# Kernel optimization log

Measured on AMD Instinct MI355X. Metric: run time of the kernel, lower is better.

Reference implementation:

```python
import jax, jax.numpy as jnp
import numpy as np

DEPTH_REF = jnp.array([28.01, 16.32], dtype=jnp.float32)
DIM_REF = jnp.array([[3.88, 1.63, 1.53], [0.84, 1.76, 0.66], [1.78, 1.52, 1.78]], dtype=jnp.float32)
TOPK = 50
DET_THRESHOLD = 0.25
PI = 3.14159265358979


def nms_hm(heat, kernel=3):
    # 3x3 max-pool NMS: keep peaks, zero everything else
    pad = (kernel - 1) // 2
    hmax = jax.lax.reduce_window(heat, -jnp.inf, jax.lax.max,
                                 (1, 1, kernel, kernel), (1, 1, 1, 1),
                                 [(0, 0), (0, 0), (pad, pad), (pad, pad)])
    return jnp.where(hmax == heat, heat, 0.0)


def select_topk(heat, K):
    B, C, H, W = heat.shape
    scores_all, inds_all = jax.lax.top_k(heat.reshape(B, C, H * W), K)  # [B,C,K]
    ys_all = (inds_all // W).astype(jnp.float32)
    xs_all = (inds_all % W).astype(jnp.float32)
    scores, inds = jax.lax.top_k(scores_all.reshape(B, C * K), K)       # [B,K] over classes
    clses = (inds // K).astype(jnp.float32)
    topk_inds = jnp.take_along_axis(inds_all.reshape(B, C * K), inds, axis=1)
    ys = jnp.take_along_axis(ys_all.reshape(B, C * K), inds, axis=1)
    xs = jnp.take_along_axis(xs_all.reshape(B, C * K), inds, axis=1)
    return scores, topk_inds, clses, ys, xs


def select_point_of_interest(index, feature_maps):
    B, Cf, H, W = feature_maps.shape
    fm = feature_maps.transpose(0, 2, 3, 1).reshape(B, H * W, Cf)
    return jnp.take_along_axis(fm, index[:, :, None], axis=1)  # [B,K,Cf]


def encode_box3d(rotys, dims, locs):
    # dims = (l, h, w); corner signs reproduce SMOKE's gather pattern
    N = rotys.shape[0]
    c, s = jnp.cos(rotys), jnp.sin(rotys)
    z, o = jnp.zeros_like(c), jnp.ones_like(c)
    ry = jnp.stack([c, z, s, z, o, z, -s, z, c], axis=1).reshape(N, 3, 3)
    sx = jnp.array([-0.5, 0.5, 0.5, 0.5, 0.5, -0.5, -0.5, -0.5], dtype=dims.dtype)
    sy = jnp.array([-1., -1., 0., 0., -1., -1., 0., 0.], dtype=dims.dtype)
    sz = jnp.array([-0.5, -0.5, -0.5, 0.5, 0.5, 0.5, 0.5, -0.5], dtype=dims.dtype)
    corners = jnp.stack([dims[:, 0:1] * sx, dims[:, 1:2] * sy, dims[:, 2:3] * sz], axis=1)  # [N,3,8]
    return jnp.einsum('nij,njk->nik', ry, corners) + locs[:, :, None]


def setup_inputs() -> dict:
    key = jax.random.key(0)
    k1, k2 = jax.random.split(key)
    B, C, H, W = 32, 3, 192, 640
    IMG_W, IMG_H = 4 * W, 4 * H
    pred_heatmap = jax.random.uniform(k1, (B, C, H, W), dtype=jnp.float32)
    pred_regression = jax.random.normal(k2, (B, 8, H, W), dtype=jnp.float32) * 0.5
    # affine image->heatmap (scale 1/4), invertible
    tm = jnp.array([[0.25, 0., 0.], [0., 0.25, 0.], [0., 0., 1.]], dtype=jnp.float32)
    trans_mat = jnp.tile(tm[None], (B, 1, 1))
    Kc = jnp.array([[721.5, 0., IMG_W / 2.], [0., 721.5, IMG_H / 2.], [0., 0., 1.]], dtype=jnp.float32)
    K_mat = jnp.tile(Kc[None], (B, 1, 1))
    img_size = jnp.tile(jnp.array([[IMG_W, IMG_H]], dtype=jnp.float32), (B, 1))
    return {"pred_heatmap": pred_heatmap, "pred_regression": pred_regression,
            "trans_mat": trans_mat, "K_mat": K_mat, "img_size": img_size}


def reference(pred_heatmap, pred_regression, trans_mat, K_mat, img_size):
    B = pred_heatmap.shape[0]
    heat = nms_hm(pred_heatmap)
    scores, inds, clses, ys, xs = select_topk(heat, TOPK)
    reg = select_point_of_interest(inds, pred_regression).reshape(-1, 8)  # [B*K,8]

    points = jnp.stack([xs.reshape(-1), ys.reshape(-1)], axis=1)          # heatmap coords
    depth_off, proj_off = reg[:, 0], reg[:, 1:3]
    dim_off, ori = reg[:, 3:6], reg[:, 6:8]
    cls_idx = clses.reshape(-1).astype(jnp.int32)

    obj_id = jnp.repeat(jnp.arange(B), TOPK)
    tm_inv = jnp.linalg.inv(trans_mat)[obj_id]   # [N,3,3]
    K_inv = jnp.linalg.inv(K_mat)[obj_id]

    # decode location: heatmap -> image -> camera frame
    proj = points + proj_off
    proj_ext = jnp.concatenate([proj, jnp.ones_like(proj[:, :1])], axis=1)
    proj_img = jnp.einsum('nij,nj->ni', tm_inv, proj_ext)                 # image-plane homog coords
    depths = depth_off * DEPTH_REF[1] + DEPTH_REF[0]
    locs = jnp.einsum('nij,nj->ni', K_inv, proj_img * depths[:, None])

    dims = jnp.exp(dim_off) * DIM_REF[cls_idx]                            # (l,h,w)
    locs = locs.at[:, 1].add(dims[:, 1] / 2)

    # decode orientation
    eps = 1e-7
    rays = jnp.arctan(locs[:, 0] / (locs[:, 2] + eps))
    alphas = jnp.arctan(ori[:, 0] / (ori[:, 1] + eps))
    alphas = jnp.where(ori[:, 1] >= 0, alphas - PI / 2, alphas + PI / 2)
    rotys = alphas + rays
    wrap = lambda a: jnp.where(a > PI, a - 2 * PI, jnp.where(a < -PI, a + 2 * PI, a))
    rotys, alphas = wrap(rotys), wrap(alphas)

    # encode 2D boxes from projected 3D corners
    corners = encode_box3d(rotys, dims, locs)                             # [N,3,8]
    proj2 = jnp.einsum('nij,njk->nik', K_mat[obj_id], corners)
    xy = proj2[:, :2] / proj2[:, 2:3]
    Wi, Hi = img_size[obj_id, 0], img_size[obj_id, 1]
    xmins = jnp.clip(xy[:, 0].min(axis=1), 0.0, Wi)
    ymins = jnp.clip(xy[:, 1].min(axis=1), 0.0, Hi)
    xmaxs = jnp.clip(xy[:, 0].max(axis=1), 0.0, Wi)
    ymaxs = jnp.clip(xy[:, 1].max(axis=1), 0.0, Hi)
    box2d = jnp.stack([xmins, ymins, xmaxs, ymaxs], axis=1)

    dims_rolled = jnp.roll(dims, -1, axis=1)                              # (h,w,l)
    result = jnp.concatenate([
        cls_idx.astype(jnp.float32)[:, None], alphas[:, None], box2d,
        dims_rolled, locs, rotys[:, None], scores.reshape(-1, 1)], axis=1)  # [B*K,14]
    keep = result[:, -1] > DET_THRESHOLD
    return jnp.where(keep[:, None], result, 0.0)
```

## Files before the change

kernel.cpp:

```cpp
#include <hip/hip_runtime.h>
#include <math.h>

#define Hd 192
#define Wd 640
#define HWp (Hd * Wd)
#define NCLS 3
#define KTOP 50
#define NB 32
#define NPL (NB * NCLS)
#define NSUB 8
#define BROWS 24
#define NCOL 40
#define NACT (NCOL * 6)
#define CAPS 512
#define CAP 2048
#define RBK 256
#define GPR 160
#define GPP (HWp / 4)
#define NMERGE (NCLS * NSUB * KTOP)
#define TH_F 0.995f
#define PI_F 3.14159265358979f

#define OFF_SSC 0
#define OFF_SPI 0x40000
#define OFF_SCNT 0x80000

__device__ inline float fmax3(float a, float b, float c) {
  return fmaxf(fmaxf(a, b), c);
}

__device__ inline unsigned long long mk_key(unsigned int bits, int idx) {
  return ((unsigned long long)bits << 32) | (unsigned int)~idx;
}

__device__ inline int bucket_of(unsigned int bits) {
  const unsigned int base = __float_as_uint(TH_F);
  if (bits <= base) return 0;
  unsigned int d = (bits - base) >> 9;
  return d > 255u ? 255 : (int)d;
}

__device__ inline unsigned long long mk_key19(unsigned int bits, int cls, int idx) {
  return ((unsigned long long)bits << 19) |
         ((unsigned long long)(2 - cls) << 17) |
         (unsigned long long)((idx ^ 0x1FFFF) & 0x1FFFF);
}

struct Row16 {
  float4 q0, q1, q2, q3;
  float l, r;
};

__device__ inline Row16 load_row16(const float* __restrict__ rp, int x0, bool valid) {
  Row16 o;
  if (valid) {
    o.q0 = *(const float4*)(rp);
    o.q1 = *(const float4*)(rp + 4);
    o.q2 = *(const float4*)(rp + 8);
    o.q3 = *(const float4*)(rp + 12);
    o.l = (x0 > 0) ? rp[-1] : -INFINITY;
    o.r = (x0 + 16 < Wd) ? rp[16] : -INFINITY;
  } else {
    o.q0.x = o.q0.y = o.q0.z = o.q0.w = -INFINITY;
    o.q1 = o.q0; o.q2 = o.q0; o.q3 = o.q0;
    o.l = -INFINITY; o.r = -INFINITY;
  }
  return o;
}

__device__ inline float4 max3v(const float4 a, const float4 b, const float4 c) {
  float4 o;
  o.x = fmax3(a.x, b.x, c.x);
  o.y = fmax3(a.y, b.y, c.y);
  o.z = fmax3(a.z, b.z, c.z);
  o.w = fmax3(a.w, b.w, c.w);
  return o;
}

template <typename F>
__device__ inline void band_scan(const float* __restrict__ hp, int band,
                                 int tid, F&& f) {
  if (tid >= NACT) return;
  const int c = tid % NCOL;
  const int rg = tid / NCOL;
  const int r0 = band * BROWS + rg * 4;
  const int x0 = c * 16;
  const float* colp = hp + x0;

  Row16 rt = load_row16(colp + (long)(r0 - 1) * Wd, x0, r0 > 0);
  Row16 rm = load_row16(colp + (long)r0 * Wd, x0, true);
#pragma unroll
  for (int j = 0; j < 4; ++j) {
    const int y = r0 + j;
    const Row16 rb = load_row16(colp + (long)(y + 1) * Wd, x0, y + 1 < Hd);

    const float cl = fmax3(rt.l, rm.l, rb.l);
    const float cr = fmax3(rt.r, rm.r, rb.r);
    const float4 c0 = max3v(rt.q0, rm.q0, rb.q0);
    const float4 c1 = max3v(rt.q1, rm.q1, rb.q1);
    const float4 c2 = max3v(rt.q2, rm.q2, rb.q2);
    const float4 c3 = max3v(rt.q3, rm.q3, rb.q3);
    const int base = y * Wd + x0;
#define EMIT(V, W0, W1, W2, J)                                       \
    if ((V) >= TH_F && (V) == fmax3((W0), (W1), (W2)))               \
      f(__float_as_uint(V), base + (J));
    EMIT(rm.q0.x, cl,   c0.x, c0.y, 0)
    EMIT(rm.q0.y, c0.x, c0.y, c0.z, 1)
    EMIT(rm.q0.z, c0.y, c0.z, c0.w, 2)
    EMIT(rm.q0.w, c0.z, c0.w, c1.x, 3)
    EMIT(rm.q1.x, c0.w, c1.x, c1.y, 4)
    EMIT(rm.q1.y, c1.x, c1.y, c1.z, 5)
    EMIT(rm.q1.z, c1.y, c1.z, c1.w, 6)
    EMIT(rm.q1.w, c1.z, c1.w, c2.x, 7)
    EMIT(rm.q2.x, c1.w, c2.x, c2.y, 8)
    EMIT(rm.q2.y, c2.x, c2.y, c2.z, 9)
    EMIT(rm.q2.z, c2.y, c2.z, c2.w, 10)
    EMIT(rm.q2.w, c2.z, c2.w, c3.x, 11)
    EMIT(rm.q3.x, c2.w, c3.x, c3.y, 12)
    EMIT(rm.q3.y, c3.x, c3.y, c3.z, 13)
    EMIT(rm.q3.z, c3.y, c3.z, c3.w, 14)
    EMIT(rm.q3.w, c3.z, c3.w, cr,   15)
#undef EMIT
    rt = rm;
    rm = rb;
  }
}

template <typename F>
__device__ inline void peaks_in_group(const float* __restrict__ p, int g, F&& f) {
  const int y = g / GPR;
  const int x0 = (g - y * GPR) * 4;
  const float* rm = p + y * Wd + x0;
  const float4 mq = *(const float4*)rm;
  const float ml = (x0 > 0) ? rm[-1] : -INFINITY;
  const float mr = (x0 + 4 < Wd) ? rm[4] : -INFINITY;
  float4 tq; float tl, tr;
  if (y > 0) {
    const float* rt = rm - Wd;
    tq = *(const float4*)rt;
    tl = (x0 > 0) ? rt[-1] : -INFINITY;
    tr = (x0 + 4 < Wd) ? rt[4] : -INFINITY;
  } else {
    tq.x = tq.y = tq.z = tq.w = -INFINITY; tl = -INFINITY; tr = -INFINITY;
  }
  float4 bq; float bl, br;
  if (y < Hd - 1) {
    const float* rb = rm + Wd;
    bq = *(const float4*)rb;
    bl = (x0 > 0) ? rb[-1] : -INFINITY;
    br = (x0 + 4 < Wd) ? rb[4] : -INFINITY;
  } else {
    bq.x = bq.y = bq.z = bq.w = -INFINITY; bl = -INFINITY; br = -INFINITY;
  }
  const float c0 = fmax3(tl, ml, bl);
  const float c1 = fmax3(tq.x, mq.x, bq.x);
  const float c2 = fmax3(tq.y, mq.y, bq.y);
  const float c3 = fmax3(tq.z, mq.z, bq.z);
  const float c4 = fmax3(tq.w, mq.w, bq.w);
  const float c5 = fmax3(tr, mr, br);
  const int base = y * Wd + x0;
  if (mq.x == fmax3(c0, c1, c2)) f(__float_as_uint(mq.x), base + 0);
  if (mq.y == fmax3(c1, c2, c3)) f(__float_as_uint(mq.y), base + 1);
  if (mq.z == fmax3(c2, c3, c4)) f(__float_as_uint(mq.z), base + 2);
  if (mq.w == fmax3(c3, c4, c5)) f(__float_as_uint(mq.w), base + 3);
}

template <typename F>
__device__ inline void for_each_peak_plane(const float* __restrict__ p, int tid,
                                           int nth, F&& f) {
  for (int g = tid; g < GPP; g += nth) peaks_in_group(p, g, f);
}

__device__ inline void inv3(const float* m, float* o) {
  float a = m[0], b = m[1], c = m[2];
  float d = m[3], e = m[4], f = m[5];
  float g = m[6], h = m[7], i = m[8];
  float A = e * i - f * h;
  float B = -(d * i - f * g);
  float C = d * h - e * g;
  float det = a * A + b * B + c * C;
  float id = 1.0f / det;
  o[0] = A * id;            o[1] = -(b * i - c * h) * id; o[2] = (b * f - c * e) * id;
  o[3] = B * id;            o[4] = (a * i - c * g) * id;  o[5] = -(a * f - c * d) * id;
  o[6] = C * id;            o[7] = -(a * h - b * g) * id; o[8] = (a * e - b * d) * id;
}

__device__ inline float wrap_pi(float a) {
  if (a > PI_F) return a - 2.0f * PI_F;
  if (a < -PI_F) return a + 2.0f * PI_F;
  return a;
}

__constant__ float DIM_REF_C[9] = {3.88f, 1.63f, 1.53f,
                                   0.84f, 1.76f, 0.66f,
                                   1.78f, 1.52f, 1.78f};

__global__ __launch_bounds__(256) void scanrank_kernel(
    const float* __restrict__ heat,
    float* __restrict__ ssc,
    int* __restrict__ spi,
    int* __restrict__ scnt) {
  const int blk = blockIdx.x;
  const int tid = threadIdx.x;
  const int plane = blk / NSUB;
  const int band = blk - plane * NSUB;
  const float* hp = heat + (size_t)plane * HWp;

  __shared__ unsigned long long s_key[CAPS];
  __shared__ unsigned long long c_key[CAPS];
  __shared__ int cnt[RBK], suf[RBK], cur[RBK];
  __shared__ int s_n, s_B, s_above, s_T;

  if (tid == 0) s_n = 0;
  __syncthreads();

  band_scan(hp, band, tid, [&](unsigned int bits, int idx) {
    int slot = atomicAdd(&s_n, 1);
    if (slot < CAPS) s_key[slot] = mk_key(bits, idx);
  });
  __syncthreads();
  int n = s_n;

  if (n > CAPS) {
    unsigned int* hist = (unsigned int*)c_key;
    const unsigned int THB = __float_as_uint(TH_F);
    for (int i = tid; i < 1024; i += 256) hist[i] = 0;
    __syncthreads();
    band_scan(hp, band, tid, [&](unsigned int bits, int idx) {
      atomicAdd(&hist[(bits - THB) >> 7], 1u);
    });
    __syncthreads();
    if (tid == 0) {
      int acc = 0, res = 0, above = 0;
      for (int q = 655; q >= 0; --q) {
        int cc = (int)hist[q];
        if (acc + cc >= KTOP) { res = q; above = acc; break; }
        acc += cc;
      }
      s_B = res; s_above = above;
    }
    __syncthreads();
    const int Bc = s_B;
    for (int i = tid; i < 1024; i += 256) hist[i] = 0;
    __syncthreads();
    band_scan(hp, band, tid, [&](unsigned int bits, int idx) {
      if ((int)((bits - THB) >> 7) == Bc)
        atomicAdd(&hist[(bits - THB) & 127], 1u);
    });
    __syncthreads();
    if (tid == 0) {
      int acc = s_above, S = 0;
      for (int sb = 127; sb >= 0; --sb) {
        int cc = (int)hist[sb];
        if (acc + cc >= KTOP) { S = sb; break; }
        acc += cc;
      }
      s_T = (int)(THB + ((unsigned int)Bc << 7) + (unsigned int)S);
      s_n = 0;
    }
    __syncthreads();
    const unsigned int T = (unsigned int)s_T;
    band_scan(hp, band, tid, [&](unsigned int bits, int idx) {
      if (bits >= T) {
        int slot = atomicAdd(&s_n, 1);
        if (slot < CAPS) s_key[slot] = mk_key(bits, idx);
      }
    });
    __syncthreads();
    n = s_n < CAPS ? s_n : CAPS;
  }

  cnt[tid] = 0;
  cur[tid] = 0;
  __syncthreads();
  for (int i = tid; i < n; i += 256)
    atomicAdd(&cnt[bucket_of((unsigned int)(s_key[i] >> 32))], 1);
  __syncthreads();
  suf[tid] = cnt[tid];
  __syncthreads();
#pragma unroll
  for (int d = 1; d < RBK; d <<= 1) {
    const int v = (tid + d < RBK) ? suf[tid + d] : 0;
    __syncthreads();
    suf[tid] += v;
    __syncthreads();
  }
  {
    const int excl = suf[tid] - cnt[tid];
    __syncthreads();
    suf[tid] = excl;
  }
  __syncthreads();
  for (int i = tid; i < n; i += 256) {
    const unsigned long long k = s_key[i];
    const int bq = bucket_of((unsigned int)(k >> 32));
    const int slot = suf[bq] + atomicAdd(&cur[bq], 1);
    c_key[slot] = k;
  }
  __syncthreads();
  float* psc = ssc + blk * 64;
  int* ppi = spi + blk * 64;
  for (int i = tid; i < n; i += 256) {
    const unsigned long long k = c_key[i];
    const int bq = bucket_of((unsigned int)(k >> 32));
    const int st = suf[bq];
    const int nb = cnt[bq];
    int rank = st;
    for (int tt = st; tt < st + nb; ++tt) rank += (c_key[tt] > k);
    if (rank < KTOP) {
      psc[rank] = __uint_as_float((unsigned int)(k >> 32));
      ppi[rank] = (int)~((unsigned int)k);
    }
  }
  for (int s2 = n + tid; s2 < KTOP; s2 += 256) {
    psc[s2] = 0.0f;
    ppi[s2] = 0;
  }
  if (tid == 0) scnt[blk] = n;
}

__global__ __launch_bounds__(256) void decode_kernel(
    const float* __restrict__ heat,
    const float* __restrict__ ssc,
    const int* __restrict__ spi,
    const int* __restrict__ scnt,
    const float* __restrict__ regr,
    const float* __restrict__ trans_mat,
    const float* __restrict__ K_mat,
    const float* __restrict__ img_size,
    float* __restrict__ out) {
  const int b = blockIdx.x;
  const int tid = threadIdx.x;

  __shared__ unsigned long long d_keys[NMERGE];
  __shared__ unsigned long long g_keys[NMERGE];
  __shared__ int cnt[RBK], suf[RBK], cur[RBK];
  __shared__ int sel[KTOP];
  __shared__ int s_ctl[NCLS * NSUB];
  __shared__ int s_ct[NCLS];
  __shared__ unsigned long long s_key[CAP];
  __shared__ unsigned long long c_key[CAP];
  __shared__ int s_fbB, s_fbAbove, s_fbT, s_fbCnt;

  if (tid < NCLS * NSUB) s_ctl[tid] = scnt[b * NCLS * NSUB + tid];
  __syncthreads();
  if (tid < NCLS) {
    int t = 0;
#pragma unroll
    for (int s = 0; s < NSUB; ++s) t += s_ctl[tid * NSUB + s];
    s_ct[tid] = t;
  }
  __syncthreads();

  for (int i = tid; i < NMERGE; i += 256) {
    const int c = i / (NSUB * KTOP);
    const int rem = i - c * (NSUB * KTOP);
    const int s = rem / KTOP;
    const int k2 = rem - s * KTOP;
    const int sb = (b * NCLS + c) * NSUB + s;
    const float v = ssc[sb * 64 + k2];
    const int idx = spi[sb * 64 + k2];
    d_keys[i] = mk_key19(__float_as_uint(v), c, idx);
  }
  __syncthreads();

  for (int c = 0; c < NCLS; ++c) {
    if (s_ct[c] < KTOP) {
      const float* hp = heat + (size_t)(b * NCLS + c) * HWp;
      unsigned int* fb_hist = (unsigned int*)c_key;
      for (int i = tid; i < 1024; i += 256) fb_hist[i] = 0;
      __syncthreads();
      for_each_peak_plane(hp, tid, 256, [&](unsigned int bits, int idx) {
        unsigned int bkt = bits >> 20; if (bkt > 1023u) bkt = 1023u;
        atomicAdd(&fb_hist[bkt], 1u);
      });
      __syncthreads();
      if (tid == 0) {
        int acc = 0, Bs = -1;
        for (int bkt = 1023; bkt >= 0; --bkt) {
          int cc = (int)fb_hist[bkt];
          if (acc + cc >= KTOP) { Bs = bkt; s_fbAbove = acc; break; }
          acc += cc;
        }
        s_fbB = Bs;
        if (Bs < 0) s_fbAbove = acc;
      }
      __syncthreads();
      const int Bs = s_fbB;
      unsigned int T;
      if (Bs < 0) {
        T = 0;
      } else {
        for (int i = tid; i < 1024; i += 256) fb_hist[i] = 0;
        __syncthreads();
        for_each_peak_plane(hp, tid, 256, [&](unsigned int bits, int idx) {
          unsigned int bkt = bits >> 20; if (bkt > 1023u) bkt = 1023u;
          if ((int)bkt == Bs) atomicAdd(&fb_hist[(bits >> 10) & 1023], 1u);
        });
        __syncthreads();
        if (tid == 0) {
          int acc = s_fbAbove, Ss = 0;
          for (int sb = 1023; sb >= 0; --sb) {
            int cc = (int)fb_hist[sb];
            if (acc + cc >= KTOP) { Ss = sb; break; }
            acc += cc;
          }
          s_fbT = (int)(((unsigned int)Bs << 20) | ((unsigned int)Ss << 10));
        }
        __syncthreads();
        T = (unsigned int)s_fbT;
      }
      if (tid == 0) s_fbCnt = 0;
      __syncthreads();
      for_each_peak_plane(hp, tid, 256, [&](unsigned int bits, int idx) {
        if (bits >= T) {
          int slot = atomicAdd(&s_fbCnt, 1);
          if (slot < CAP) s_key[slot] = mk_key(bits, idx);
        }
      });
      __syncthreads();
      const int M = s_fbCnt < CAP ? s_fbCnt : CAP;
      cnt[tid] = 0; cur[tid] = 0;
      __syncthreads();
      for (int i = tid; i < M; i += 256)
        atomicAdd(&cnt[bucket_of((unsigned int)(s_key[i] >> 32))], 1);
      __syncthreads();
      suf[tid] = cnt[tid];
      __syncthreads();
#pragma unroll
      for (int d = 1; d < RBK; d <<= 1) {
        const int v = (tid + d < RBK) ? suf[tid + d] : 0;
        __syncthreads();
        suf[tid] += v;
        __syncthreads();
      }
      {
        const int excl = suf[tid] - cnt[tid];
        __syncthreads();
        suf[tid] = excl;
      }
      __syncthreads();
      for (int i = tid; i < M; i += 256) {
        const unsigned long long k = s_key[i];
        const int bq = bucket_of((unsigned int)(k >> 32));
        const int slot = suf[bq] + atomicAdd(&cur[bq], 1);
        c_key[slot] = k;
      }
      __syncthreads();
      for (int i = tid; i < NSUB * KTOP; i += 256)
        d_keys[c * (NSUB * KTOP) + i] = mk_key19(0u, c, 0);
      __syncthreads();
      for (int i = tid; i < M; i += 256) {
        const unsigned long long k = c_key[i];
        const int bq = bucket_of((unsigned int)(k >> 32));
        const int st = suf[bq];
        const int nb = cnt[bq];
        int rank = st;
        for (int tt = st; tt < st + nb; ++tt) rank += (c_key[tt] > k);
        if (rank < KTOP)
          d_keys[c * (NSUB * KTOP) + rank] =
              mk_key19((unsigned int)(k >> 32), c, (int)~((unsigned int)k));
      }
      __syncthreads();
    }
  }

  cnt[tid] = 0;
  cur[tid] = 0;
  __syncthreads();
  for (int i = tid; i < NMERGE; i += 256)
    atomicAdd(&cnt[bucket_of((unsigned int)(d_keys[i] >> 19))], 1);
  __syncthreads();
  suf[tid] = cnt[tid];
  __syncthreads();
#pragma unroll
  for (int d = 1; d < RBK; d <<= 1) {
    const int v = (tid + d < RBK) ? suf[tid + d] : 0;
    __syncthreads();
    suf[tid] += v;
    __syncthreads();
  }
  {
    const int excl = suf[tid] - cnt[tid];
    __syncthreads();
    suf[tid] = excl;
  }
  __syncthreads();
  for (int i = tid; i < NMERGE; i += 256) {
    const unsigned long long k = d_keys[i];
    const int bq = bucket_of((unsigned int)(k >> 19));
    const int slot = suf[bq] + atomicAdd(&cur[bq], 1);
    g_keys[slot] = k;
  }
  __syncthreads();
  for (int i = tid; i < NMERGE; i += 256) {
    const unsigned long long k = g_keys[i];
    const int bq = bucket_of((unsigned int)(k >> 19));
    const int st = suf[bq];
    if (st >= KTOP) continue;
    const int nb = cnt[bq];
    int rank = st;
    for (int tt = st; tt < st + nb; ++tt) rank += (g_keys[tt] > k);
    if (rank < KTOP) sel[rank] = i;
  }
  __syncthreads();

  if (tid < KTOP) {
    const unsigned long long k = g_keys[sel[tid]];
    const float score = __uint_as_float((unsigned int)(k >> 19));
    const int cls = 2 - (int)((k >> 17) & 3);
    const int ind = ((int)(k & 0x1FFFF)) ^ 0x1FFFF;
    const float ys = (float)(ind / Wd);
    const float xs = (float)(ind - (ind / Wd) * Wd);

    const float* rb = regr + (size_t)b * 8 * HWp + ind;
    const float r0 = rb[0 * HWp], r1 = rb[1 * HWp], r2 = rb[2 * HWp], r3 = rb[3 * HWp];
    const float r4 = rb[4 * HWp], r5 = rb[5 * HWp], r6 = rb[6 * HWp], r7 = rb[7 * HWp];

    float tm[9], km[9], tmi[9], kmi[9];
#pragma unroll
    for (int q = 0; q < 9; ++q) { tm[q] = trans_mat[b * 9 + q]; km[q] = K_mat[b * 9 + q]; }
    inv3(tm, tmi);
    inv3(km, kmi);

    const float px = xs + r1, py = ys + r2;
    const float gx = tmi[0] * px + tmi[1] * py + tmi[2];
    const float gy = tmi[3] * px + tmi[4] * py + tmi[5];
    const float gz = tmi[6] * px + tmi[7] * py + tmi[8];
    const float depth = r0 * 16.32f + 28.01f;
    const float qx = gx * depth, qy = gy * depth, qz = gz * depth;
    const float lx = kmi[0] * qx + kmi[1] * qy + kmi[2] * qz;
    float ly = kmi[3] * qx + kmi[4] * qy + kmi[5] * qz;
    const float lz = kmi[6] * qx + kmi[7] * qy + kmi[8] * qz;

    const float d0 = expf(r3) * DIM_REF_C[cls * 3 + 0];
    const float d1 = expf(r4) * DIM_REF_C[cls * 3 + 1];
    const float d2 = expf(r5) * DIM_REF_C[cls * 3 + 2];
    ly += d1 * 0.5f;

    const float ray = atanf(lx / (lz + 1e-7f));
    float alpha = atanf(r6 / (r7 + 1e-7f));
    alpha += (r7 >= 0.0f) ? -PI_F * 0.5f : PI_F * 0.5f;
    const float roty = wrap_pi(alpha + ray);
    alpha = wrap_pi(alpha);

    const float SX[8] = {-0.5f, 0.5f, 0.5f, 0.5f, 0.5f, -0.5f, -0.5f, -0.5f};
    const float SY[8] = {-1.0f, -1.0f, 0.0f, 0.0f, -1.0f, -1.0f, 0.0f, 0.0f};
    const float SZ[8] = {-0.5f, -0.5f, -0.5f, 0.5f, 0.5f, 0.5f, 0.5f, -0.5f};
    const float cr = cosf(roty), sr = sinf(roty);
    float minx = INFINITY, maxx = -INFINITY, miny = INFINITY, maxy = -INFINITY;
#pragma unroll
    for (int j = 0; j < 8; ++j) {
      const float ax = d0 * SX[j], ay = d1 * SY[j], az = d2 * SZ[j];
      const float cx = cr * ax + sr * az + lx;
      const float cy = ay + ly;
      const float cz = -sr * ax + cr * az + lz;
      const float ppx = km[0] * cx + km[1] * cy + km[2] * cz;
      const float ppy = km[3] * cx + km[4] * cy + km[5] * cz;
      const float ppz = km[6] * cx + km[7] * cy + km[8] * cz;
      const float X = ppx / ppz, Y = ppy / ppz;
      minx = fminf(minx, X); maxx = fmaxf(maxx, X);
      miny = fminf(miny, Y); maxy = fmaxf(maxy, Y);
    }
    const float Wi = img_size[b * 2 + 0], Hi = img_size[b * 2 + 1];
    const float xmin = fminf(fmaxf(minx, 0.0f), Wi);
    const float ymin = fminf(fmaxf(miny, 0.0f), Hi);
    const float xmax = fminf(fmaxf(maxx, 0.0f), Wi);
    const float ymax = fminf(fmaxf(maxy, 0.0f), Hi);

    float* o = out + (size_t)(b * KTOP + tid) * 14;
    if (score > 0.25f) {
      o[0] = (float)cls; o[1] = alpha;
      o[2] = xmin; o[3] = ymin; o[4] = xmax; o[5] = ymax;
      o[6] = d1; o[7] = d2; o[8] = d0;
      o[9] = lx; o[10] = ly; o[11] = lz;
      o[12] = roty; o[13] = score;
    } else {
#pragma unroll
      for (int q = 0; q < 14; ++q) o[q] = 0.0f;
    }
  }
}


extern "C" void kernel_launch(void* const* d_in, const int* in_sizes, int n_in,
                              void* d_out, int out_size, void* d_ws, size_t ws_size,
                              hipStream_t stream) {
  const float* heat = (const float*)d_in[0];
  const float* regr = (const float*)d_in[1];
  const float* tmat = (const float*)d_in[2];
  const float* kmat = (const float*)d_in[3];
  const float* isz = (const float*)d_in[4];

  char* ws = (char*)d_ws;
  float* ssc = (float*)(ws + OFF_SSC);
  int* spi = (int*)(ws + OFF_SPI);
  int* scnt = (int*)(ws + OFF_SCNT);

  scanrank_kernel<<<NPL * NSUB, 256, 0, stream>>>(heat, ssc, spi, scnt);
  decode_kernel<<<NB, 256, 0, stream>>>(heat, ssc, spi, scnt,
                                        regr, tmat, kmat, isz,
                                        (float*)d_out);
}
```

Before: 200.7 us.

## Replace bucket sort ranking with direct rank counting and wave-shuffle threshold select

In the scan kernel, the bucket histogram, prefix scan and scatter before ranking are removed, and each candidate is ranked by comparing against all n keys (up to CAPS). In the decode merge, the block-wide Hillis-Steele suffix scan is replaced with a wave-shuffle suffix sum that finds the threshold bucket. Only keys at or above that bucket are compacted, then ranked by all-pairs comparison. This removes many __syncthreads barriers and scatter passes, at the cost of O(n^2) comparisons when candidate counts are large.

New measurement: 201.7 us. No clear change (+0.5%).

```diff
diff --git a/kernel.cpp b/kernel.cpp
--- a/kernel.cpp
+++ b/kernel.cpp
@@ -208,7 +208,6 @@
 
   __shared__ unsigned long long s_key[CAPS];
   __shared__ unsigned long long c_key[CAPS];
-  __shared__ int cnt[RBK], suf[RBK], cur[RBK];
   __shared__ int s_n, s_B, s_above, s_T;
 
   if (tid == 0) s_n = 0;
@@ -270,43 +269,13 @@
     n = s_n < CAPS ? s_n : CAPS;
   }
 
-  cnt[tid] = 0;
-  cur[tid] = 0;
-  __syncthreads();
-  for (int i = tid; i < n; i += 256)
-    atomicAdd(&cnt[bucket_of((unsigned int)(s_key[i] >> 32))], 1);
-  __syncthreads();
-  suf[tid] = cnt[tid];
-  __syncthreads();
-#pragma unroll
-  for (int d = 1; d < RBK; d <<= 1) {
-    const int v = (tid + d < RBK) ? suf[tid + d] : 0;
-    __syncthreads();
-    suf[tid] += v;
-    __syncthreads();
-  }
-  {
-    const int excl = suf[tid] - cnt[tid];
-    __syncthreads();
-    suf[tid] = excl;
-  }
-  __syncthreads();
-  for (int i = tid; i < n; i += 256) {
-    const unsigned long long k = s_key[i];
-    const int bq = bucket_of((unsigned int)(k >> 32));
-    const int slot = suf[bq] + atomicAdd(&cur[bq], 1);
-    c_key[slot] = k;
-  }
-  __syncthreads();
   float* psc = ssc + blk * 64;
   int* ppi = spi + blk * 64;
   for (int i = tid; i < n; i += 256) {
-    const unsigned long long k = c_key[i];
-    const int bq = bucket_of((unsigned int)(k >> 32));
-    const int st = suf[bq];
-    const int nb = cnt[bq];
-    int rank = st;
-    for (int tt = st; tt < st + nb; ++tt) rank += (c_key[tt] > k);
+    const unsigned long long k = s_key[i];
+    int rank = 0;
+#pragma unroll 4
+    for (int j = 0; j < n; ++j) rank += (s_key[j] > k);
     if (rank < KTOP) {
       psc[rank] = __uint_as_float((unsigned int)(k >> 32));
       ppi[rank] = (int)~((unsigned int)k);
@@ -338,6 +307,8 @@
   __shared__ int sel[KTOP];
   __shared__ int s_ctl[NCLS * NSUB];
   __shared__ int s_ct[NCLS];
+  __shared__ int wsum[4];
+  __shared__ int s_bstar, s_ns;
   __shared__ unsigned long long s_key[CAP];
   __shared__ unsigned long long c_key[CAP];
   __shared__ int s_fbB, s_fbAbove, s_fbT, s_fbCnt;
@@ -466,41 +437,45 @@
   }
 
   cnt[tid] = 0;
-  cur[tid] = 0;
+  if (tid == 0) { s_bstar = 0; s_ns = 0; }
   __syncthreads();
   for (int i = tid; i < NMERGE; i += 256)
     atomicAdd(&cnt[bucket_of((unsigned int)(d_keys[i] >> 19))], 1);
   __syncthreads();
-  suf[tid] = cnt[tid];
-  __syncthreads();
-#pragma unroll
-  for (int d = 1; d < RBK; d <<= 1) {
-    const int v = (tid + d < RBK) ? suf[tid + d] : 0;
-    __syncthreads();
-    suf[tid] += v;
-    __syncthreads();
-  }
   {
-    const int excl = suf[tid] - cnt[tid];
-    __syncthreads();
-    suf[tid] = excl;
-  }
-  __syncthreads();
+    int v = cnt[tid];
+    const int lane = tid & 63;
+#pragma unroll
+    for (int d = 1; d < 64; d <<= 1) {
+      int t = __shfl_down(v, d);
+      if (lane + d < 64) v += t;
+    }
+    if (lane == 0) wsum[tid >> 6] = v;
+    __syncthreads();
+    int add = 0;
+    const int w = tid >> 6;
+#pragma unroll
+    for (int ww = 1; ww < 4; ++ww)
+      if (ww > w) add += wsum[ww];
+    const int suffix = v + add;
+    if (suffix >= KTOP) atomicMax(&s_bstar, tid);
+  }
+  __syncthreads();
+  const int bstar = s_bstar;
   for (int i = tid; i < NMERGE; i += 256) {
     const unsigned long long k = d_keys[i];
-    const int bq = bucket_of((unsigned int)(k >> 19));
-    const int slot = suf[bq] + atomicAdd(&cur[bq], 1);
-    g_keys[slot] = k;
-  }
-  __syncthreads();
-  for (int i = tid; i < NMERGE; i += 256) {
+    if (bucket_of((unsigned int)(k >> 19)) >= bstar) {
+      const int slot = atomicAdd(&s_ns, 1);
+      g_keys[slot] = k;
+    }
+  }
+  __syncthreads();
+  const int nsv = s_ns;
+  for (int i = tid; i < nsv; i += 256) {
     const unsigned long long k = g_keys[i];
-    const int bq = bucket_of((unsigned int)(k >> 19));
-    const int st = suf[bq];
-    if (st >= KTOP) continue;
-    const int nb = cnt[bq];
-    int rank = st;
-    for (int tt = st; tt < st + nb; ++tt) rank += (g_keys[tt] > k);
+    int rank = 0;
+#pragma unroll 4
+    for (int j = 0; j < nsv; ++j) rank += (g_keys[j] > k);
     if (rank < KTOP) sel[rank] = i;
   }
   __syncthreads();
```
